# Kernel optimization log

Hardware: AMD Instinct MI355X
Metric: run time of the kernel (lower is better)

## Reference

```python
import jax, jax.numpy as jnp
import numpy as np

B, N, D = 4, 2048, 768
H, HD = 12, 64  # num_heads, head_dims
SCALE = HD ** (-0.5)


def setup_inputs() -> dict:
    key = jax.random.key(0)
    k1, k2, k3, k4, k5 = jax.random.split(key, 5)
    s = 0.02
    return {
        "x": jax.random.normal(k1, (B, N, D), dtype=jnp.float32),
        "W_qkv": jax.random.normal(k2, (D, 3 * H * HD), dtype=jnp.float32) * s,
        "b_qkv": jax.random.normal(k3, (3 * H * HD,), dtype=jnp.float32) * s,
        "W_proj": jax.random.normal(k4, (H * HD, H * HD), dtype=jnp.float32) * s,
        "b_proj": jax.random.normal(k5, (H * HD,), dtype=jnp.float32) * s,
    }


def reference(x, W_qkv, b_qkv, W_proj, b_proj):
    b, n, d = x.shape
    qkv = x @ W_qkv + b_qkv                      # [B,N,3*H*HD]
    qkv = qkv.reshape(b, n, 3, H, HD).transpose(2, 0, 3, 1, 4)  # [3,B,H,N,HD]
    q, k, v = qkv[0], qkv[1], qkv[2]
    # NOTE non-standard order: scores = k @ q^T, softmax, THEN scale
    scores = jnp.einsum("bhnd,bhmd->bhnm", k, q)  # [B,H,N,N]
    attn = jax.nn.softmax(scores, axis=-1) * SCALE
    out = jnp.einsum("bhnm,bhmd->bhnd", attn, v)  # [B,H,N,HD]
    out = out.transpose(0, 2, 1, 3).reshape(b, n, H * HD)
    return out @ W_proj + b_proj
```

## Files before the change

kernel.cpp:

```cpp
#include <hip/hip_runtime.h>
#include <stdint.h>

#define NB_TOK 8192
#define DMODEL 768
#define NHEAD 12
#define HDIM 64
#define QKV3 2304
#define SEQ 2048
#define NBATCH 4
#define SCALE_F 0.125f
#define LOG2E 1.44269504f

typedef _Float16 f16;
typedef __attribute__((ext_vector_type(2))) __fp16 hf16x2;
typedef __attribute__((ext_vector_type(4))) _Float16 f16x4;
typedef __attribute__((ext_vector_type(8))) _Float16 f16x8;
typedef __attribute__((ext_vector_type(4))) float f32x4;
typedef __attribute__((ext_vector_type(16))) float f32x16;

__device__ __forceinline__ void gload_lds16(const void* g, void* l) {
  __builtin_amdgcn_global_load_lds(
      (const __attribute__((address_space(1))) unsigned int*)g,
      (__attribute__((address_space(3))) unsigned int*)l, 16, 0, 0);
}

__device__ __forceinline__ float fast_exp2(float x) {
  return __builtin_amdgcn_exp2f(x);
}

__global__ __launch_bounds__(256) void cvt_f32_f16_k(const float* __restrict__ in,
                                                     f16* __restrict__ out) {
  const int i = (blockIdx.x * 256 + threadIdx.x) * 4;
  const float4 v = *reinterpret_cast<const float4*>(in + i);
  f16x4 o;
  o[0] = (f16)v.x; o[1] = (f16)v.y; o[2] = (f16)v.z; o[3] = (f16)v.w;
  *reinterpret_cast<f16x4*>(out + i) = o;
}

__global__ __launch_bounds__(256) void transpose_cvt_k(const float* __restrict__ in,
                                                       f16* __restrict__ out,
                                                       int R, int C) {
  const int idx = blockIdx.x * 256 + threadIdx.x;
  const int c = idx / R, r = idx - c * R;
  out[idx] = (f16)in[r * C + c];
}

template <int MODE>
__global__ __launch_bounds__(256) void gemm128_k(
    const f16* __restrict__ A, const f16* __restrict__ Bt,
    const float* __restrict__ bias, int K,
    f16* __restrict__ Qf, f16* __restrict__ Kf, f16* __restrict__ Vf,
    float* __restrict__ Of) {
  __shared__ __align__(16) f16 As[3][128 * 32];
  __shared__ __align__(16) f16 Bs[3][128 * 32];
  const int tid = threadIdx.x;
  const int w = tid >> 6, l = tid & 63;
  const int lr = l >> 2, lc = l & 3;
  const int nwg = gridDim.x * gridDim.y;
  const int lid = blockIdx.y * gridDim.x + blockIdx.x;
  const int wg = (lid & 7) * (nwg >> 3) + (lid >> 3);
  const int bm = (wg / gridDim.x) * 128, bn = (wg % gridDim.x) * 128;
  const f16* ga = A + (size_t)(bm + lr) * K + lc * 8;
  const f16* gb = Bt + (size_t)(bn + lr) * K + lc * 8;
  const int wr = (w >> 1) * 64, wc = (w & 1) * 64;
  const int fr = l & 15, fk = (l >> 4) * 8;

  auto stage = [&](int bb, int kt) {
    gload_lds16(ga + (size_t)(w * 16) * K + kt, &As[bb][(w * 16) * 32]);
    gload_lds16(ga + (size_t)((w + 4) * 16) * K + kt, &As[bb][((w + 4) * 16) * 32]);
    gload_lds16(gb + (size_t)(w * 16) * K + kt, &Bs[bb][(w * 16) * 32]);
    gload_lds16(gb + (size_t)((w + 4) * 16) * K + kt, &Bs[bb][((w + 4) * 16) * 32]);
  };

  f32x4 acc[4][4] = {};
  stage(0, 0);
  if (32 < K) stage(1, 32);
  int cur = 0;
  for (int kt = 0; kt < K; kt += 32) {
    if (kt + 64 < K) stage((cur + 2) % 3, kt + 64);
    if (kt + 64 < K)      asm volatile("s_waitcnt vmcnt(8)" ::: "memory");
    else if (kt + 32 < K) asm volatile("s_waitcnt vmcnt(4)" ::: "memory");
    else                  asm volatile("s_waitcnt vmcnt(0)" ::: "memory");
    __builtin_amdgcn_s_barrier();
    f16x8 af[4], bfrag[4];
#pragma unroll
    for (int mi = 0; mi < 4; mi++)
      af[mi] = *reinterpret_cast<const f16x8*>(&As[cur][(wr + mi * 16 + fr) * 32 + fk]);
#pragma unroll
    for (int ni = 0; ni < 4; ni++)
      bfrag[ni] = *reinterpret_cast<const f16x8*>(&Bs[cur][(wc + ni * 16 + fr) * 32 + fk]);
#pragma unroll
    for (int mi = 0; mi < 4; mi++)
#pragma unroll
      for (int ni = 0; ni < 4; ni++)
        acc[mi][ni] = __builtin_amdgcn_mfma_f32_16x16x32_f16(af[mi], bfrag[ni],
                                                             acc[mi][ni], 0, 0, 0);
    __builtin_amdgcn_s_barrier();
    cur = (cur + 1) % 3;
  }
  const int rgrp = (l >> 4) * 4;
#pragma unroll
  for (int ni = 0; ni < 4; ni++) {
    const int j = bn + wc + ni * 16 + fr;
    const float bb = bias[j];
    if (MODE == 0) {
      const int s = j / DMODEL;
      const int rem = j - s * DMODEL;
      const int h = rem >> 6, hd = rem & 63;
      f16* dqk = (s == 0) ? Qf : Kf;
      const float scale = (s == 1) ? LOG2E : 1.0f;
#pragma unroll
      for (int mi = 0; mi < 4; mi++)
#pragma unroll
        for (int r = 0; r < 4; r++) {
          const int m = bm + wr + mi * 16 + rgrp + r;
          const int bidx = m >> 11, n2 = m & 2047;
          const f16 hv = (f16)((acc[mi][ni][r] + bb) * scale);
          const size_t bbase = (size_t)(bidx * NHEAD + h) * (SEQ * HDIM);
          if (s < 2) {
            const int mc = n2 >> 5, kt = hd >> 4;
            const int lane = (n2 & 31) + ((hd >> 3) & 1) * 32;
            dqk[bbase + (size_t)(((mc * 4 + kt) << 9) + (lane << 3) + (hd & 7))] = hv;
          } else {
            const int mc16 = n2 >> 4, g = hd >> 5;
            const int lane = (hd & 31) + ((n2 >> 3) & 1) * 32;
            Vf[bbase + (size_t)((((mc16 << 1) + g) << 9) + (lane << 3) + (n2 & 7))] = hv;
          }
        }
    } else {
#pragma unroll
      for (int mi = 0; mi < 4; mi++)
#pragma unroll
        for (int r = 0; r < 4; r++) {
          const int m = bm + wr + mi * 16 + rgrp + r;
          Of[(size_t)m * DMODEL + j] = acc[mi][ni][r] + bb;
        }
    }
  }
}

__device__ __forceinline__ void attn_step(const f16x8 (&fk)[4], const f16x8 (&fv)[4],
                                          const f16x8 (&fq)[4], f32x16& o0, f32x16& o1,
                                          float (&den)[4]) {
  f32x16 acc;
#pragma unroll
  for (int r = 0; r < 16; r++) acc[r] = -12.0f;
#pragma unroll
  for (int kt = 0; kt < 4; kt++)
    acc = __builtin_amdgcn_mfma_f32_32x32x16_f16(fk[kt], fq[kt], acc, 0, 0, 0);
  float p[16];
#pragma unroll
  for (int r = 0; r < 16; r++) {
    p[r] = fast_exp2(acc[r]);
    den[r & 3] += p[r];
  }
  union PW { hf16x2 h; uint32_t w; };
  uint32_t u[8];
#pragma unroll
  for (int i = 0; i < 8; i++) {
    PW t; t.h = __builtin_amdgcn_cvt_pkrtz(p[2 * i], p[2 * i + 1]);
    u[i] = t.w;
  }
  asm("v_permlane32_swap_b32 %0, %1" : "+v"(u[0]), "+v"(u[2]));
  asm("v_permlane32_swap_b32 %0, %1" : "+v"(u[1]), "+v"(u[3]));
  asm("v_permlane32_swap_b32 %0, %1" : "+v"(u[4]), "+v"(u[6]));
  asm("v_permlane32_swap_b32 %0, %1" : "+v"(u[5]), "+v"(u[7]));
  union FR { uint32_t w[4]; f16x8 v; };
  FR fa0, fa1;
  fa0.w[0] = u[0]; fa0.w[1] = u[1]; fa0.w[2] = u[2]; fa0.w[3] = u[3];
  fa1.w[0] = u[4]; fa1.w[1] = u[5]; fa1.w[2] = u[6]; fa1.w[3] = u[7];
  o0 = __builtin_amdgcn_mfma_f32_32x32x16_f16(fa0.v, fv[0], o0, 0, 0, 0);
  o0 = __builtin_amdgcn_mfma_f32_32x32x16_f16(fa1.v, fv[1], o0, 0, 0, 0);
  o1 = __builtin_amdgcn_mfma_f32_32x32x16_f16(fa0.v, fv[2], o1, 0, 0, 0);
  o1 = __builtin_amdgcn_mfma_f32_32x32x16_f16(fa1.v, fv[3], o1, 0, 0, 0);
}

__global__ __launch_bounds__(256, 3) void attn_k(const f16* __restrict__ Qf,
                                                 const f16* __restrict__ Kf,
                                                 const f16* __restrict__ Vf,
                                                 f16* __restrict__ AO) {
  __shared__ __align__(16) f16 kv[2][4][4][512];
  const int lid = blockIdx.y * 16 + blockIdx.x;
  const int wg = (lid & 7) * 96 + (lid >> 3);
  const int rb = wg & 15;
  const int bh = wg >> 4;
  const int b = bh / NHEAD, h = bh - b * NHEAD;
  const int w = threadIdx.x >> 6, l = threadIdx.x & 63;
  const int ln = l & 31, hi = l >> 5;
  const size_t base = (size_t)bh * SEQ * HDIM;
  const f16* Qfp = Qf + base;
  const f16* Kfp = Kf + base;
  const f16* Vfp = Vf + base;
  const int n0 = rb * 128 + w * 32;

  f16x8 fq[4];
#pragma unroll
  for (int kt = 0; kt < 4; kt++)
    fq[kt] = *reinterpret_cast<const f16x8*>(
        Kfp + ((((n0 >> 5) * 4 + kt) << 9) + (l << 3)));

  auto stage = [&](int bb, int it) {
    if (w < 2) {
      const int mc = 2 * it + w;
#pragma unroll
      for (int c = 0; c < 4; c++)
        gload_lds16(Qfp + (((mc * 4 + c) << 9) + (l << 3)), &kv[bb][w][c][0]);
    } else {
      const int m16 = 4 * it + (w - 2) * 2;
#pragma unroll
      for (int c = 0; c < 4; c++)
        gload_lds16(Vfp + ((((m16 + (c & 1)) * 2 + (c >> 1)) << 9) + (l << 3)),
                    &kv[bb][w][c][0]);
    }
  };
  auto ldfrag = [&](f16x8 (&fr)[4], int bb, int tile) {
#pragma unroll
    for (int c = 0; c < 4; c++)
      fr[c] = *reinterpret_cast<const f16x8*>(&kv[bb][tile][c][l << 3]);
  };

  f32x16 o0 = {}, o1 = {};
  float den[4] = {0.f, 0.f, 0.f, 0.f};
  stage(0, 0);
  asm volatile("s_waitcnt vmcnt(0)" ::: "memory");
  __builtin_amdgcn_s_barrier();
  int cur = 0;
  for (int it = 0; it < SEQ / 64; it++) {
    if (it + 1 < SEQ / 64) stage(cur ^ 1, it + 1);
    f16x8 fkA[4], fvA[4], fkB[4], fvB[4];
    ldfrag(fkA, cur, 0); ldfrag(fvA, cur, 2);
    attn_step(fkA, fvA, fq, o0, o1, den);
    ldfrag(fkB, cur, 1); ldfrag(fvB, cur, 3);
    attn_step(fkB, fvB, fq, o0, o1, den);
    asm volatile("s_waitcnt vmcnt(0)" ::: "memory");
    __builtin_amdgcn_s_barrier();
    cur ^= 1;
  }
  float d = (den[0] + den[1]) + (den[2] + den[3]);
  d += __shfl_xor(d, 32, 64);
  const float inv = SCALE_F / d;
#pragma unroll
  for (int r = 0; r < 16; r++) {
    const int nr = (r & 3) + 8 * (r >> 2) + 4 * hi;
    const float invr = __shfl(inv, nr, 64);
    const size_t row = ((size_t)(b * SEQ + n0 + nr)) * DMODEL + h * HDIM;
    AO[row + ln] = (f16)(o0[r] * invr);
    AO[row + 32 + ln] = (f16)(o1[r] * invr);
  }
}

extern "C" void kernel_launch(void* const* d_in, const int* in_sizes, int n_in,
                              void* d_out, int out_size, void* d_ws, size_t ws_size,
                              hipStream_t stream) {
  const float* x = (const float*)d_in[0];
  const float* Wqkv = (const float*)d_in[1];
  const float* bqkv = (const float*)d_in[2];
  const float* Wproj = (const float*)d_in[3];
  const float* bproj = (const float*)d_in[4];
  float* outp = (float*)d_out;

  f16* xh = (f16*)d_ws;
  f16* AO = xh;
  f16* wqkvt = xh + (size_t)NB_TOK * DMODEL;
  f16* wprojt = wqkvt + (size_t)QKV3 * DMODEL;
  f16* Qf = wprojt + (size_t)DMODEL * DMODEL;
  f16* Kf = Qf + (size_t)NBATCH * NHEAD * SEQ * HDIM;
  f16* Vf = Kf + (size_t)NBATCH * NHEAD * SEQ * HDIM;

  cvt_f32_f16_k<<<(NB_TOK * DMODEL) / 1024, 256, 0, stream>>>(x, xh);
  transpose_cvt_k<<<(QKV3 * DMODEL) / 256, 256, 0, stream>>>(Wqkv, wqkvt, DMODEL, QKV3);
  transpose_cvt_k<<<(DMODEL * DMODEL) / 256, 256, 0, stream>>>(Wproj, wprojt, DMODEL, DMODEL);
  gemm128_k<0><<<dim3(QKV3 / 128, NB_TOK / 128), 256, 0, stream>>>(
      xh, wqkvt, bqkv, DMODEL, Qf, Kf, Vf, nullptr);
  attn_k<<<dim3(SEQ / 128, NBATCH * NHEAD), 256, 0, stream>>>(Qf, Kf, Vf, AO);
  gemm128_k<1><<<dim3(DMODEL / 128, NB_TOK / 128), 256, 0, stream>>>(
      AO, wprojt, bproj, DMODEL, nullptr, nullptr, nullptr, outp);
}
```

Baseline: 166.7 us.

## Use 256x256-tile, 8-wave GEMM with swizzled LDS for QKV projection

Replaces the 128x128 QKV projection GEMM with a new 256x256-tile kernel using 512 threads, a K-step of 64, XOR-swizzled LDS layout loaded via global_load_lds, double buffering with explicit vmcnt waits, and raised priority around the MFMA blocks. Larger tiles raise arithmetic intensity and cut global traffic per FLOP. The grid shrinks to 288 workgroups, which may leave compute units underfilled or unbalanced, and the kernel uses a large LDS footprint. The old MODE 0 epilogue is removed from the template.

New measurement: 179.2 us. +7.5%, slower.

```diff
diff --git a/kernel.cpp b/kernel.cpp
--- a/kernel.cpp
+++ b/kernel.cpp
@@ -43,6 +43,114 @@
   const int idx = blockIdx.x * 256 + threadIdx.x;
   const int c = idx / R, r = idx - c * R;
   out[idx] = (f16)in[r * C + c];
+}
+
+__global__ __launch_bounds__(512, 2) void gemm256_k(
+    const f16* __restrict__ A, const f16* __restrict__ Bt,
+    const float* __restrict__ bias,
+    f16* __restrict__ Qf, f16* __restrict__ Kf, f16* __restrict__ Vf) {
+  __shared__ __align__(16) f16 Ls[2][4][8192];
+  const int tid = threadIdx.x;
+  const int w = tid >> 6, l = tid & 63;
+  const int warp_m = w >> 2, warp_n = w & 3;
+  const int fr = l & 15;
+  const int K = DMODEL;
+  const int lid = blockIdx.y * gridDim.x + blockIdx.x;
+  const int wg = (lid & 7) * 36 + (lid >> 3);
+  const int bm = (wg / 9) * 256, bn = (wg % 9) * 256;
+
+  auto stageHalf = [&](int buf, int q, int tile) {
+#pragma unroll
+    for (int j = 0; j < 2; j++) {
+      const int slot = j * 512 + tid;
+      const int row = slot >> 3, cg = slot & 7;
+      const f16* base = (q < 2) ? A + (size_t)(bm + (q & 1) * 128 + row) * K
+                                : Bt + (size_t)(bn + (q & 1) * 128 + row) * K;
+      gload_lds16(base + tile * 64 + ((cg ^ (row & 7)) << 3),
+                  &Ls[buf][q][(j * 512 + (tid & ~63)) * 8]);
+    }
+  };
+
+  f32x4 acc[8][4] = {};
+  stageHalf(0, 0, 0); stageHalf(0, 1, 0); stageHalf(0, 2, 0); stageHalf(0, 3, 0);
+  const int cq = l >> 4;
+  for (int it = 0; it < 6; it++) {
+#pragma unroll
+    for (int half = 0; half < 2; half++) {
+      const int par = half;
+      f16x8 bfr[8];
+#pragma unroll
+      for (int q = 0; q < 4; q++) {
+        const int ts = 2 * it + 1 + half;
+        const bool st = (ts < 12);
+        if (st) stageHalf(par ^ 1, q, ts);
+        if (q == 0) {
+          if (st) asm volatile("s_waitcnt vmcnt(2)" ::: "memory");
+          else    asm volatile("s_waitcnt vmcnt(0)" ::: "memory");
+          __builtin_amdgcn_s_barrier();
+#pragma unroll
+          for (int ni = 0; ni < 4; ni++)
+#pragma unroll
+            for (int ks = 0; ks < 2; ks++) {
+              const int rl = (warp_n & 1) * 64 + ni * 16 + fr;
+              const int cg = ks * 4 + cq;
+              bfr[ni * 2 + ks] = *reinterpret_cast<const f16x8*>(
+                  &Ls[par][2 + (warp_n >> 1)][(rl * 8 + (cg ^ (rl & 7))) * 8]);
+            }
+        }
+        f16x8 af[4];
+#pragma unroll
+        for (int dm = 0; dm < 2; dm++)
+#pragma unroll
+          for (int ks = 0; ks < 2; ks++) {
+            const int rl = (2 * q + dm) * 16 + fr;
+            const int cg = ks * 4 + cq;
+            af[dm * 2 + ks] = *reinterpret_cast<const f16x8*>(
+                &Ls[par][warp_m][(rl * 8 + (cg ^ (rl & 7))) * 8]);
+          }
+        __builtin_amdgcn_s_setprio(1);
+#pragma unroll
+        for (int dm = 0; dm < 2; dm++)
+#pragma unroll
+          for (int ni = 0; ni < 4; ni++)
+#pragma unroll
+            for (int ks = 0; ks < 2; ks++)
+              acc[2 * q + dm][ni] = __builtin_amdgcn_mfma_f32_16x16x32_f16(
+                  af[dm * 2 + ks], bfr[ni * 2 + ks], acc[2 * q + dm][ni], 0, 0, 0);
+        __builtin_amdgcn_s_setprio(0);
+        __builtin_amdgcn_s_barrier();
+      }
+    }
+  }
+  const int rgrp = (l >> 4) * 4;
+#pragma unroll
+  for (int ni = 0; ni < 4; ni++) {
+    const int j = bn + warp_n * 64 + ni * 16 + fr;
+    const float bb = bias[j];
+    const int s = j / DMODEL;
+    const int rem = j - s * DMODEL;
+    const int h = rem >> 6, hd = rem & 63;
+    f16* dqk = (s == 0) ? Qf : Kf;
+    const float scale = (s == 1) ? LOG2E : 1.0f;
+#pragma unroll
+    for (int mi = 0; mi < 8; mi++)
+#pragma unroll
+      for (int r = 0; r < 4; r++) {
+        const int m = bm + warp_m * 128 + mi * 16 + rgrp + r;
+        const int bidx = m >> 11, n2 = m & 2047;
+        const f16 hv = (f16)((acc[mi][ni][r] + bb) * scale);
+        const size_t bbase = (size_t)(bidx * NHEAD + h) * (SEQ * HDIM);
+        if (s < 2) {
+          const int mc = n2 >> 5, kt = hd >> 4;
+          const int lane = (n2 & 31) + ((hd >> 3) & 1) * 32;
+          dqk[bbase + (size_t)(((mc * 4 + kt) << 9) + (lane << 3) + (hd & 7))] = hv;
+        } else {
+          const int mc16 = n2 >> 4, g = hd >> 5;
+          const int lane = (hd & 31) + ((n2 >> 3) & 1) * 32;
+          Vf[bbase + (size_t)((((mc16 << 1) + g) << 9) + (lane << 3) + (n2 & 7))] = hv;
+        }
+      }
+  }
 }
 
 template <int MODE>
@@ -103,39 +211,13 @@
   for (int ni = 0; ni < 4; ni++) {
     const int j = bn + wc + ni * 16 + fr;
     const float bb = bias[j];
-    if (MODE == 0) {
-      const int s = j / DMODEL;
-      const int rem = j - s * DMODEL;
-      const int h = rem >> 6, hd = rem & 63;
-      f16* dqk = (s == 0) ? Qf : Kf;
-      const float scale = (s == 1) ? LOG2E : 1.0f;
-#pragma unroll
-      for (int mi = 0; mi < 4; mi++)
-#pragma unroll
-        for (int r = 0; r < 4; r++) {
-          const int m = bm + wr + mi * 16 + rgrp + r;
-          const int bidx = m >> 11, n2 = m & 2047;
-          const f16 hv = (f16)((acc[mi][ni][r] + bb) * scale);
-          const size_t bbase = (size_t)(bidx * NHEAD + h) * (SEQ * HDIM);
-          if (s < 2) {
-            const int mc = n2 >> 5, kt = hd >> 4;
-            const int lane = (n2 & 31) + ((hd >> 3) & 1) * 32;
-            dqk[bbase + (size_t)(((mc * 4 + kt) << 9) + (lane << 3) + (hd & 7))] = hv;
-          } else {
-            const int mc16 = n2 >> 4, g = hd >> 5;
-            const int lane = (hd & 31) + ((n2 >> 3) & 1) * 32;
-            Vf[bbase + (size_t)((((mc16 << 1) + g) << 9) + (lane << 3) + (n2 & 7))] = hv;
-          }
-        }
-    } else {
-#pragma unroll
-      for (int mi = 0; mi < 4; mi++)
-#pragma unroll
-        for (int r = 0; r < 4; r++) {
-          const int m = bm + wr + mi * 16 + rgrp + r;
-          Of[(size_t)m * DMODEL + j] = acc[mi][ni][r] + bb;
-        }
-    }
+#pragma unroll
+    for (int mi = 0; mi < 4; mi++)
+#pragma unroll
+      for (int r = 0; r < 4; r++) {
+        const int m = bm + wr + mi * 16 + rgrp + r;
+        Of[(size_t)m * DMODEL + j] = acc[mi][ni][r] + bb;
+      }
   }
 }
 
@@ -270,8 +352,7 @@
   cvt_f32_f16_k<<<(NB_TOK * DMODEL) / 1024, 256, 0, stream>>>(x, xh);
   transpose_cvt_k<<<(QKV3 * DMODEL) / 256, 256, 0, stream>>>(Wqkv, wqkvt, DMODEL, QKV3);
   transpose_cvt_k<<<(DMODEL * DMODEL) / 256, 256, 0, stream>>>(Wproj, wprojt, DMODEL, DMODEL);
-  gemm128_k<0><<<dim3(QKV3 / 128, NB_TOK / 128), 256, 0, stream>>>(
-      xh, wqkvt, bqkv, DMODEL, Qf, Kf, Vf, nullptr);
+  gemm256_k<<<dim3(9, 32), 512, 0, stream>>>(xh, wqkvt, bqkv, Qf, Kf, Vf);
   attn_k<<<dim3(SEQ / 128, NBATCH * NHEAD), 256, 0, stream>>>(Qf, Kf, Vf, AO);
   gemm128_k<1><<<dim3(DMODEL / 128, NB_TOK / 128), 256, 0, stream>>>(
       AO, wprojt, bproj, DMODEL, nullptr, nullptr, nullptr, outp);
```
